# Kernel optimization log

Hardware: AMD Instinct MI355X
Metric: run time of the kernel (lower is better)

## Reference

```python
import jax, jax.numpy as jnp
import numpy as np

N_NODES = 50000


def _sage_max(x, src, dst, W_l, b_l, W_r):
    # gather neighbor (source) features, scatter-max to destination nodes
    msgs = x[src]                                   # [E, F]
    agg = jax.ops.segment_max(msgs, dst, num_segments=N_NODES)  # [N, F], -inf for empty
    agg = jnp.where(jnp.isneginf(agg), 0.0, agg)    # PyG fills isolated nodes with 0
    return agg @ W_l + b_l + x @ W_r                # lin_l(aggr) + lin_r(x)


def setup_inputs() -> dict:
    key = jax.random.key(0)
    ks = jax.random.split(key, 9)
    F_IN, H, OUT, E, EL = 128, 256, 32, 800000, 200000
    x = jax.random.normal(ks[0], (N_NODES, F_IN), dtype=jnp.float32)
    edge_index = jax.random.randint(ks[1], (2, E), 0, N_NODES, dtype=jnp.int64)
    edge_label_index = jax.random.randint(ks[2], (2, EL), 0, N_NODES, dtype=jnp.int64)
    s1 = 1.0 / np.sqrt(F_IN)
    s2 = 1.0 / np.sqrt(H)
    W1_l = jax.random.normal(ks[3], (F_IN, H), dtype=jnp.float32) * s1
    b1 = jnp.zeros((H,), dtype=jnp.float32)
    W1_r = jax.random.normal(ks[4], (F_IN, H), dtype=jnp.float32) * s1
    W2_l = jax.random.normal(ks[5], (H, OUT), dtype=jnp.float32) * s2
    b2 = jnp.zeros((OUT,), dtype=jnp.float32)
    W2_r = jax.random.normal(ks[6], (H, OUT), dtype=jnp.float32) * s2
    return {"x": x, "edge_index": edge_index, "edge_label_index": edge_label_index,
            "W1_l": W1_l, "b1": b1, "W1_r": W1_r,
            "W2_l": W2_l, "b2": b2, "W2_r": W2_r}


def reference(x, edge_index, edge_label_index, W1_l, b1, W1_r, W2_l, b2, W2_r):
    src, dst = edge_index[0], edge_index[1]
    # encode (eval mode: dropout is identity)
    h = jax.nn.relu(_sage_max(x, src, dst, W1_l, b1, W1_r))
    z = _sage_max(h, src, dst, W2_l, b2, W2_r)       # [N, 32]
    # decode: dot product between endpoint embeddings
    s = z[edge_label_index[0]]
    d = z[edge_label_index[1]]
    return jnp.sum(s * d, axis=-1)                   # [E_label]
```

## Files before the change

### kernel.cpp

```cpp
#include <hip/hip_runtime.h>
#include <hip/hip_bf16.h>
#include <math.h>

#define N_NODES 50000
#define NBKT 196
#define BSH 8
#define TILE2 4096
#define CAP 64
#define P2CAP 5888
#define SCAN_FLAG 0x40000000
#define ZSTRIDE 1600000

typedef __attribute__((ext_vector_type(8))) short short8;
typedef __attribute__((ext_vector_type(4))) float f32x4;

static __device__ __forceinline__ float b2f(unsigned int u16) {
    union { unsigned int i; float f; } c; c.i = u16 << 16; return c.f;
}
static __device__ __forceinline__ unsigned int fbits(float f) {
    union { float f; unsigned int i; } c; c.f = f; return c.i;
}
static __device__ __forceinline__ unsigned short f2b_rne(float f) {
    unsigned int u = fbits(f);
    u += 0x7fff + ((u >> 16) & 1);
    return (unsigned short)(u >> 16);
}

static __device__ __forceinline__ unsigned char quant8(float v) {
    int q = (int)(v * 15.9375f + 0.5f);
    return (unsigned char)min(q, 255);
}

static __device__ __forceinline__ unsigned char q8x(float v) {
    int q = __float2int_rn(v * 21.333334f) + 128;
    return (unsigned char)min(max(q, 0), 255);
}

static __device__ __forceinline__ short8 dq8(uint2 v8) {
    short8 r;
#pragma unroll
    for (int bi = 0; bi < 4; ++bi)
        r[bi] = (short)f2b_rne((float)((v8.x >> (8 * bi)) & 255u) * 0.0627451f);
#pragma unroll
    for (int bi = 0; bi < 4; ++bi)
        r[4 + bi] = (short)f2b_rne((float)((v8.y >> (8 * bi)) & 255u) * 0.0627451f);
    return r;
}

#define BYTEMAX16(V) do {                                                             \
    m[0]  = max(m[0],  (int)((V).x & 0xFF));                                          \
    m[1]  = max(m[1],  (int)(((V).x >> 8) & 0xFF));                                   \
    m[2]  = max(m[2],  (int)(((V).x >> 16) & 0xFF));                                  \
    m[3]  = max(m[3],  (int)((V).x >> 24));                                           \
    m[4]  = max(m[4],  (int)((V).y & 0xFF));                                          \
    m[5]  = max(m[5],  (int)(((V).y >> 8) & 0xFF));                                   \
    m[6]  = max(m[6],  (int)(((V).y >> 16) & 0xFF));                                  \
    m[7]  = max(m[7],  (int)((V).y >> 24));                                           \
    m[8]  = max(m[8],  (int)((V).z & 0xFF));                                          \
    m[9]  = max(m[9],  (int)(((V).z >> 8) & 0xFF));                                   \
    m[10] = max(m[10], (int)(((V).z >> 16) & 0xFF));                                  \
    m[11] = max(m[11], (int)((V).z >> 24));                                           \
    m[12] = max(m[12], (int)((V).w & 0xFF));                                          \
    m[13] = max(m[13], (int)(((V).w >> 8) & 0xFF));                                   \
    m[14] = max(m[14], (int)(((V).w >> 16) & 0xFF));                                  \
    m[15] = max(m[15], (int)((V).w >> 24));                                           \
} while (0)


__global__ __launch_bounds__(256) void k_prepbin(
        const float* __restrict__ x, unsigned short* __restrict__ xb,
        unsigned char* __restrict__ x8,
        const float* __restrict__ W1l, const float* __restrict__ W1r, unsigned short* __restrict__ wt1,
        const float* __restrict__ W2l, const float* __restrict__ W2r, unsigned short* __restrict__ wt2,
        const int* __restrict__ src, const int* __restrict__ dst, int E,
        uint2* __restrict__ tmp, int* __restrict__ cnts, int ntile) {
    __shared__ int cnt[256], sstart[256], lcur[256];
    __shared__ uint2 stage[TILE2];
    const int CX = (N_NODES * 128 / 4) / 256;
    const int CW = CX + 320;
    int b = blockIdx.x, t = threadIdx.x;
    if (b < CX) {
        int i = b * 256 + t;
        float4 v = *(const float4*)(x + (size_t)i * 4);
        ushort4 o;
        o.x = f2b_rne(v.x); o.y = f2b_rne(v.y); o.z = f2b_rne(v.z); o.w = f2b_rne(v.w);
        *(ushort4*)(xb + (size_t)i * 4) = o;
        uchar4 c8;
        c8.x = q8x(v.x); c8.y = q8x(v.y); c8.z = q8x(v.z); c8.w = q8x(v.w);
        *(uchar4*)(x8 + (size_t)i * 4) = c8;
    } else if (b < CX + 256) {
        int i = (b - CX) * 256 + t;
        int n = i >> 8, k = i & 255;
        float v = (k < 128) ? W1l[(size_t)k * 256 + n] : W1r[(size_t)(k - 128) * 256 + n];
        wt1[(size_t)n * 256 + k] = f2b_rne(v);
    } else if (b < CW) {
        int i = (b - CX - 256) * 256 + t;
        int n = i >> 9, k = i & 511;
        float v = (k < 256) ? W2l[(size_t)k * 32 + n] : W2r[(size_t)(k - 256) * 32 + n];
        wt2[(size_t)n * 512 + k] = f2b_rne(v);
    } else {
        int tb = b - CW;
        int e0 = tb * TILE2;
        int tilecnt = min(TILE2, E - e0);
        if (tilecnt <= 0) return;
        cnt[t] = 0;
        __syncthreads();
        if (tilecnt == TILE2) {
            for (int i = 4 * t; i < TILE2; i += 1024) {
                int4 d = *(const int4*)(dst + e0 + i);
                atomicAdd(&cnt[d.x >> BSH], 1);
                atomicAdd(&cnt[d.y >> BSH], 1);
                atomicAdd(&cnt[d.z >> BSH], 1);
                atomicAdd(&cnt[d.w >> BSH], 1);
            }
        } else {
            for (int i = t; i < tilecnt; i += 256)
                atomicAdd(&cnt[dst[e0 + i] >> BSH], 1);
        }
        __syncthreads();
        int cv = cnt[t];
        sstart[t] = cv;
        __syncthreads();
        for (int off = 1; off < 256; off <<= 1) {
            int add = (t >= off) ? sstart[t - off] : 0;
            __syncthreads();
            sstart[t] += add;
            __syncthreads();
        }
        int mystart = sstart[t] - cv;
        __syncthreads();
        sstart[t] = mystart;
        lcur[t] = mystart;
        __syncthreads();
        if (tilecnt == TILE2) {
            for (int i = 4 * t; i < TILE2; i += 1024) {
                int4 d = *(const int4*)(dst + e0 + i);
                int4 s = *(const int4*)(src + e0 + i);
                int q0 = atomicAdd(&lcur[d.x >> BSH], 1); stage[q0] = (uint2){(unsigned)s.x, (unsigned)d.x};
                int q1 = atomicAdd(&lcur[d.y >> BSH], 1); stage[q1] = (uint2){(unsigned)s.y, (unsigned)d.y};
                int q2 = atomicAdd(&lcur[d.z >> BSH], 1); stage[q2] = (uint2){(unsigned)s.z, (unsigned)d.z};
                int q3 = atomicAdd(&lcur[d.w >> BSH], 1); stage[q3] = (uint2){(unsigned)s.w, (unsigned)d.w};
            }
        } else {
            for (int i = t; i < tilecnt; i += 256) {
                int d = dst[e0 + i];
                int s = src[e0 + i];
                int q = atomicAdd(&lcur[d >> BSH], 1);
                uint2 p; p.x = (unsigned)s; p.y = (unsigned)d;
                stage[q] = p;
            }
        }
        __syncthreads();
        if (t < NBKT) cnts[(size_t)t * ntile + tb] = cnt[t];
        for (int i = t; i < tilecnt; i += 256) {
            uint2 p = stage[i];
            int bk = (int)(p.y >> BSH);
            tmp[((size_t)bk * ntile + tb) * CAP + (i - sstart[bk])] = p;
        }
    }
}


__global__ __launch_bounds__(256) void k_bin2(const uint2* __restrict__ tmp,
        const int* __restrict__ cnts, int* __restrict__ pub,
        int* __restrict__ rowptr, int* __restrict__ esrc, int N, int E, int ntile) {
    __shared__ int sc[256], toff[260], nodecnt[256], lcur[256];
    __shared__ int stage[P2CAP];
    __shared__ int shsum[4];
    int k = blockIdx.x, t = threadIdx.x;
    int grp = t >> 5, lane32 = t & 31;

    int c = (t < ntile) ? cnts[(size_t)k * ntile + t] : 0;
    sc[t] = c;
    __syncthreads();
    for (int off = 1; off < 256; off <<= 1) {
        int add = (t >= off) ? sc[t - off] : 0;
        __syncthreads();
        sc[t] += add;
        __syncthreads();
    }
    if (t < ntile) toff[t] = sc[t] - c;
    if (t == 255) toff[ntile] = sc[255];
    __syncthreads();
    int total = toff[ntile];

    if (t == 255) atomicExch(&pub[k], SCAN_FLAG | total);
    int v = 0;
    if (t < k) {
        int val;
        do { val = atomicOr(&pub[t], 0); } while (!(val & SCAN_FLAG) || (val & 0x80000000));
        v = val & (SCAN_FLAG - 1);
    }
#pragma unroll
    for (int off = 32; off >= 1; off >>= 1) v += __shfl_xor(v, off);
    if ((t & 63) == 0) shsum[t >> 6] = v;
    nodecnt[t] = 0;
    __syncthreads();
    int base = shsum[0] + shsum[1] + shsum[2] + shsum[3];

    for (int tile = grp; tile < ntile; tile += 8) {
        int tc = toff[tile + 1] - toff[tile];
        for (int e = lane32; e < tc; e += 32) {
            uint2 p = tmp[((size_t)k * ntile + tile) * CAP + e];
            atomicAdd(&nodecnt[(int)p.y & 255], 1);
        }
    }
    __syncthreads();

    int nc = nodecnt[t];
    sc[t] = nc;
    __syncthreads();
    for (int off = 1; off < 256; off <<= 1) {
        int add = (t >= off) ? sc[t - off] : 0;
        __syncthreads();
        sc[t] += add;
        __syncthreads();
    }
    int ex = sc[t] - nc;
    int node = (k << BSH) + t;
    if (node < N) rowptr[node] = base + ex;
    if (node == N) rowptr[N] = E;
    lcur[t] = ex;
    __syncthreads();

    if (total <= P2CAP) {
        for (int tile = grp; tile < ntile; tile += 8) {
            int tc = toff[tile + 1] - toff[tile];
            for (int e = lane32; e < tc; e += 32) {
                uint2 p = tmp[((size_t)k * ntile + tile) * CAP + e];
                int q = atomicAdd(&lcur[(int)p.y & 255], 1);
                stage[q] = (int)p.x;
            }
        }
        __syncthreads();
        for (int i = t; i < total; i += 256)
            esrc[base + i] = stage[i];
    } else {
        for (int tile = grp; tile < ntile; tile += 8) {
            int tc = toff[tile + 1] - toff[tile];
            for (int e = lane32; e < tc; e += 32) {
                uint2 p = tmp[((size_t)k * ntile + tile) * CAP + e];
                int q = atomicAdd(&lcur[(int)p.y & 255], 1);
                esrc[base + q] = (int)p.x;
            }
        }
    }
}


__global__ __launch_bounds__(256) void k_seg_max1(const unsigned char* __restrict__ feat8,
        const int* __restrict__ rowptr, const int* __restrict__ esrc,
        unsigned short* __restrict__ out) {
    int w = threadIdx.x >> 6, t = threadIdx.x & 63;
    int n = blockIdx.x * 4 + w;
    int lane8 = t & 7, sub = t >> 3;
    int beg = rowptr[n], end = rowptr[n + 1];
    int m[16];
#pragma unroll
    for (int k = 0; k < 16; ++k) m[k] = 0;
    for (int base = beg; base < end; base += 64) {
        int cnt = min(64, end - base);
        int vidx = (base + t < end) ? __builtin_nontemporal_load(&esrc[base + t]) : 0;
        for (int j = 0; j < cnt; j += 32) {
            int lim = cnt - j;
            if (lim > 16) {
                uint4 v[4];
#pragma unroll
                for (int u = 0; u < 4; ++u) {
                    int e = min(j + 8 * u + sub, cnt - 1);
                    int s = __shfl(vidx, e);
                    v[u] = *(const uint4*)(feat8 + (size_t)s * 128 + lane8 * 16);
                }
#pragma unroll
                for (int u = 0; u < 4; ++u) BYTEMAX16(v[u]);
            } else if (lim > 8) {
                uint4 v[2];
#pragma unroll
                for (int u = 0; u < 2; ++u) {
                    int e = min(j + 8 * u + sub, cnt - 1);
                    int s = __shfl(vidx, e);
                    v[u] = *(const uint4*)(feat8 + (size_t)s * 128 + lane8 * 16);
                }
#pragma unroll
                for (int u = 0; u < 2; ++u) BYTEMAX16(v[u]);
            } else {
                int e = min(j + sub, cnt - 1);
                int s = __shfl(vidx, e);
                uint4 v0 = *(const uint4*)(feat8 + (size_t)s * 128 + lane8 * 16);
                BYTEMAX16(v0);
            }
        }
    }
#pragma unroll
    for (int k = 0; k < 16; ++k) {
        m[k] = max(m[k], __shfl_xor(m[k], 8));
        m[k] = max(m[k], __shfl_xor(m[k], 16));
        m[k] = max(m[k], __shfl_xor(m[k], 32));
    }
    if (sub == 0) {
        unsigned int pk[8];
#pragma unroll
        for (int k = 0; k < 8; ++k) {
            float f0 = (beg == end) ? 0.f : (float)(m[2 * k]     - 128) * 0.046875f;
            float f1 = (beg == end) ? 0.f : (float)(m[2 * k + 1] - 128) * 0.046875f;
            pk[k] = (fbits(f0) >> 16) | (fbits(f1) & 0xffff0000u);
        }
        uint4 a, b;
        a.x = pk[0]; a.y = pk[1]; a.z = pk[2]; a.w = pk[3];
        b.x = pk[4]; b.y = pk[5]; b.z = pk[6]; b.w = pk[7];
        *(uint4*)(out + (size_t)n * 128 + lane8 * 16) = a;
        *(uint4*)(out + (size_t)n * 128 + lane8 * 16 + 8) = b;
    }
}


__global__ __launch_bounds__(256) void k_seg_max2(const unsigned char* __restrict__ feat8,
        const int* __restrict__ rowptr, const int* __restrict__ esrc,
        unsigned char* __restrict__ out8) {
    int w = threadIdx.x >> 6, t = threadIdx.x & 63;
    int n = blockIdx.x * 4 + w;
    int lane16 = t & 15, sub = t >> 4;
    int beg = rowptr[n], end = rowptr[n + 1];
    int m[16];
#pragma unroll
    for (int k = 0; k < 16; ++k) m[k] = 0;
    for (int base = beg; base < end; base += 64) {
        int cnt = min(64, end - base);
        int vidx = (base + t < end) ? __builtin_nontemporal_load(&esrc[base + t]) : 0;
        for (int j = 0; j < cnt; j += 32) {
            int lim = cnt - j;
            if (lim > 16) {
                uint4 v[8];
#pragma unroll
                for (int u = 0; u < 8; ++u) {
                    int e = min(j + 4 * u + sub, cnt - 1);
                    int s = __shfl(vidx, e);
                    v[u] = *(const uint4*)(feat8 + (size_t)s * 256 + lane16 * 16);
                }
#pragma unroll
                for (int u = 0; u < 8; ++u) BYTEMAX16(v[u]);
            } else if (lim > 8) {
                uint4 v[4];
#pragma unroll
                for (int u = 0; u < 4; ++u) {
                    int e = min(j + 4 * u + sub, cnt - 1);
                    int s = __shfl(vidx, e);
                    v[u] = *(const uint4*)(feat8 + (size_t)s * 256 + lane16 * 16);
                }
#pragma unroll
                for (int u = 0; u < 4; ++u) BYTEMAX16(v[u]);
            } else {
                uint4 v[2];
#pragma unroll
                for (int u = 0; u < 2; ++u) {
                    int e = min(j + 4 * u + sub, cnt - 1);
                    int s = __shfl(vidx, e);
                    v[u] = *(const uint4*)(feat8 + (size_t)s * 256 + lane16 * 16);
                }
#pragma unroll
                for (int u = 0; u < 2; ++u) BYTEMAX16(v[u]);
            }
        }
    }
#pragma unroll
    for (int k = 0; k < 16; ++k) {
        m[k] = max(m[k], __shfl_xor(m[k], 16));
        m[k] = max(m[k], __shfl_xor(m[k], 32));
    }
    if (sub == 0) {
        uint4 p;
        p.x = m[0]  | (m[1]  << 8) | (m[2]  << 16) | (m[3]  << 24);
        p.y = m[4]  | (m[5]  << 8) | (m[6]  << 16) | (m[7]  << 24);
        p.z = m[8]  | (m[9]  << 8) | (m[10] << 16) | (m[11] << 24);
        p.w = m[12] | (m[13] << 8) | (m[14] << 16) | (m[15] << 24);
        *(uint4*)(out8 + (size_t)n * 256 + lane16 * 16) = p;
    }
}


#define STAGE(bi, K0) do {                                                            \
    const unsigned short* Ab_ = ((K0) < 128) ? A0 : A1;                               \
    int kab_ = ((K0) & 127) * 2;                                                      \
    int kbb_ = (K0) * 2;                                                              \
    _Pragma("unroll")                                                                 \
    for (int ii = 0; ii < 2; ++ii) {                                                  \
        int c_ = ii * 256 + tid;                                                      \
        int r_ = c_ >> 2, gs_ = (c_ & 3) ^ (r_ & 3);                                  \
        const char* ga_ = (const char*)Ab_ + (size_t)(m0 + r_) * 256 + kab_ + gs_ * 16; \
        __builtin_amdgcn_global_load_lds(                                             \
            (const __attribute__((address_space(1))) void*)ga_,                       \
            (__attribute__((address_space(3))) void*)((char*)(SH + (bi) * 4096) + (ii * 256 + (tid & ~63)) * 16), \
            16, 0, 0);                                                                \
        const char* gb_ = (const char*)WT + (size_t)(n0 + r_) * 512 + kbb_ + gs_ * 16; \
        __builtin_amdgcn_global_load_lds(                                             \
            (const __attribute__((address_space(1))) void*)gb_,                       \
            (__attribute__((address_space(3))) void*)((char*)(SH + 12288 + (bi) * 4096) + (ii * 256 + (tid & ~63)) * 16), \
            16, 0, 0);                                                                \
    }                                                                                 \
} while (0)

#define VMCNT8() asm volatile("s_waitcnt vmcnt(8)" ::: "memory")
#define VMCNT6() asm volatile("s_waitcnt vmcnt(6)" ::: "memory")
#define VMCNT4() asm volatile("s_waitcnt vmcnt(4)" ::: "memory")
#define VMCNT3() asm volatile("s_waitcnt vmcnt(3)" ::: "memory")
#define VMCNT0() asm volatile("s_waitcnt vmcnt(0)" ::: "memory")
#define SBAR() do { __builtin_amdgcn_sched_barrier(0); __builtin_amdgcn_s_barrier(); __builtin_amdgcn_sched_barrier(0); } while (0)

#define COMPUTE(bi) do {                                                              \
    const short* Asb_ = SH + (bi) * 4096;                                             \
    const short* Bsb_ = SH + 12288 + (bi) * 4096;                                     \
    short8 a_[4], b_[4];                                                              \
    _Pragma("unroll")                                                                 \
    for (int i = 0; i < 4; ++i) {                                                     \
        int r_ = wr * 64 + i * 16 + lane16;                                           \
        a_[i] = *(const short8*)((const char*)Asb_ + r_ * 64 + ((q ^ (r_ & 3)) << 4)); \
    }                                                                                 \
    _Pragma("unroll")                                                                 \
    for (int j = 0; j < 4; ++j) {                                                     \
        int c_ = wc * 64 + j * 16 + lane16;                                           \
        b_[j] = *(const short8*)((const char*)Bsb_ + c_ * 64 + ((q ^ (c_ & 3)) << 4)); \
    }                                                                                 \
    _Pragma("unroll")                                                                 \
    for (int i = 0; i < 4; ++i)                                                       \
        _Pragma("unroll")                                                             \
        for (int j = 0; j < 4; ++j)                                                   \
            acc[i][j] = __builtin_amdgcn_mfma_f32_16x16x32_bf16(a_[i], b_[j], acc[i][j], 0, 0, 0); \
} while (0)

__global__ __launch_bounds__(256) void k_lin1_mfma(
        const unsigned short* __restrict__ A0, const unsigned short* __restrict__ A1,
        const unsigned short* __restrict__ WT, const float* __restrict__ bias,
        const unsigned short* __restrict__ WT2, float* __restrict__ zpart,
        unsigned char* __restrict__ H8, int M) {
    __shared__ __align__(16) short SH[24576];
    short* Hs = SH;

    int tid = threadIdx.x;
    int m0 = blockIdx.y * 128, n0 = blockIdx.x * 128;
    int L = tid & 63, wv = tid >> 6;
    int wr = wv >> 1, wc = wv & 1;
    int lane16 = L & 15, q = L >> 4;

    f32x4 acc[4][4];
#pragma unroll
    for (int i = 0; i < 4; ++i)
#pragma unroll
        for (int j = 0; j < 4; ++j) acc[i][j] = (f32x4){0.f, 0.f, 0.f, 0.f};

    STAGE(0, 0);
    STAGE(1, 32);
    STAGE(2, 64);

    VMCNT8(); SBAR(); COMPUTE(0); SBAR(); STAGE(0, 96);
    VMCNT8(); SBAR(); COMPUTE(1); SBAR(); STAGE(1, 128);
    VMCNT8(); SBAR(); COMPUTE(2); SBAR(); STAGE(2, 160);
    VMCNT8(); SBAR(); COMPUTE(0); SBAR(); STAGE(0, 192);
    VMCNT8(); SBAR(); COMPUTE(1); SBAR(); STAGE(1, 224);
    VMCNT8(); SBAR(); COMPUTE(2);
    VMCNT4(); SBAR(); COMPUTE(0);
    VMCNT0(); SBAR(); COMPUTE(1);

    __syncthreads();

#pragma unroll
    for (int i = 0; i < 4; ++i) {
#pragma unroll
        for (int r = 0; r < 4; ++r) {
            int lrow = wr * 64 + i * 16 + q * 4 + r;
            int row = m0 + lrow;
#pragma unroll
            for (int j = 0; j < 4; ++j) {
                int lcol = wc * 64 + j * 16 + lane16;
                int col = n0 + lcol;
                float v = fmaxf(acc[i][j][r] + bias[col], 0.f);
                Hs[lrow * 136 + lcol] = (short)f2b_rne(v);
                if (row < M) H8[(size_t)row * 256 + col] = quant8(v);
            }
        }
    }
    __syncthreads();

    f32x4 acc2[2][2];
#pragma unroll
    for (int i = 0; i < 2; ++i)
#pragma unroll
        for (int j = 0; j < 2; ++j) acc2[i][j] = (f32x4){0.f, 0.f, 0.f, 0.f};
#pragma unroll
    for (int kk = 0; kk < 4; ++kk) {
        short8 a2[2], b2[2];
#pragma unroll
        for (int i = 0; i < 2; ++i)
            a2[i] = *(const short8*)&Hs[(wv * 32 + i * 16 + lane16) * 136 + kk * 32 + q * 8];
#pragma unroll
        for (int j = 0; j < 2; ++j)
            b2[j] = *(const short8*)(WT2 + (size_t)(j * 16 + lane16) * 512 + 256 + n0 + kk * 32 + q * 8);
#pragma unroll
        for (int i = 0; i < 2; ++i)
#pragma unroll
            for (int j = 0; j < 2; ++j)
                acc2[i][j] = __builtin_amdgcn_mfma_f32_16x16x32_bf16(a2[i], b2[j], acc2[i][j], 0, 0, 0);
    }
    float* zp = zpart + (size_t)blockIdx.x * ZSTRIDE;
#pragma unroll
    for (int i = 0; i < 2; ++i) {
#pragma unroll
        for (int r = 0; r < 4; ++r) {
            int row = m0 + wv * 32 + i * 16 + q * 4 + r;
            if (row >= M) continue;
#pragma unroll
            for (int j = 0; j < 2; ++j) {
                int col = j * 16 + lane16;
                zp[(size_t)row * 32 + col] = acc2[i][j][r];
            }
        }
    }
}


#define STAGE2(bi, T) do {                                                            \
    _Pragma("unroll")                                                                 \
    for (int ii = 0; ii < 2; ++ii) {                                                  \
        int off_ = (ii * 256 + tid) * 16;                                             \
        int r_ = off_ >> 6, c_ = off_ & 63;                                           \
        const char* ga_ = (const char*)A8 + (size_t)(m0 + r_) * 256 + (T) * 64 + c_;  \
        __builtin_amdgcn_global_load_lds(                                             \
            (const __attribute__((address_space(1))) void*)ga_,                       \
            (__attribute__((address_space(3))) void*)(SH8 + (bi) * 8192 + (ii * 256 + (tid & ~63)) * 16), \
            16, 0, 0);                                                                \
    }                                                                                 \
    {                                                                                 \
        int off_ = tid * 16;                                                          \
        int r_ = off_ >> 7, c_ = off_ & 127;                                          \
        const char* gb_ = (const char*)WT + (size_t)r_ * 1024 + (T) * 128 + c_;       \
        __builtin_amdgcn_global_load_lds(                                             \
            (const __attribute__((address_space(1))) void*)gb_,                       \
            (__attribute__((address_space(3))) void*)(SH8 + 24576 + (bi) * 4096 + (tid & ~63) * 16), \
            16, 0, 0);                                                                \
    }                                                                                 \
} while (0)

#define COMPUTE2(bi) do {                                                             \
    const unsigned char* As_ = (const unsigned char*)SH8 + (bi) * 8192;               \
    const char* Bs_ = SH8 + 24576 + (bi) * 4096;                                      \
    _Pragma("unroll")                                                                 \
    for (int kk = 0; kk < 64; kk += 32) {                                             \
        short8 a_[2], b_[2];                                                          \
        _Pragma("unroll")                                                             \
        for (int i = 0; i < 2; ++i) {                                                 \
            uint2 va_ = *(const uint2*)(As_ + (wv * 32 + i * 16 + lane16) * 64 + kk + q * 8); \
            a_[i] = dq8(va_);                                                         \
        }                                                                             \
        _Pragma("unroll")                                                             \
        for (int j = 0; j < 2; ++j)                                                   \
            b_[j] = *(const short8*)(Bs_ + (j * 16 + lane16) * 128 + (kk + q * 8) * 2); \
        _Pragma("unroll")                                                             \
        for (int i = 0; i < 2; ++i)                                                   \
            _Pragma("unroll")                                                         \
            for (int j = 0; j < 2; ++j)                                               \
                acc[i][j] = __builtin_amdgcn_mfma_f32_16x16x32_bf16(a_[i], b_[j], acc[i][j], 0, 0, 0); \
    }                                                                                 \
} while (0)

__global__ __launch_bounds__(256) void k_lin2_mfma(
        const unsigned char* __restrict__ A8,
        const unsigned short* __restrict__ WT, const float* __restrict__ bias,
        const float* __restrict__ zpart, float* __restrict__ Z, int M) {
    __shared__ __align__(16) char SH8[36864];

    int tid = threadIdx.x;
    int m0 = blockIdx.x * 128;
    int L = tid & 63, wv = tid >> 6;
    int lane16 = L & 15, q = L >> 4;

    f32x4 acc[2][2];
#pragma unroll
    for (int i = 0; i < 2; ++i)
#pragma unroll
        for (int j = 0; j < 2; ++j) acc[i][j] = (f32x4){0.f, 0.f, 0.f, 0.f};

    STAGE2(0, 0);
    STAGE2(1, 1);
    STAGE2(2, 2);

    VMCNT6(); SBAR(); COMPUTE2(0); SBAR(); STAGE2(0, 3);
    VMCNT6(); SBAR(); COMPUTE2(1);
    VMCNT3(); SBAR(); COMPUTE2(2);
    VMCNT0(); SBAR(); COMPUTE2(0);

#pragma unroll
    for (int i = 0; i < 2; ++i) {
#pragma unroll
        for (int r = 0; r < 4; ++r) {
            int row = m0 + wv * 32 + i * 16 + q * 4 + r;
            if (row >= M) continue;
#pragma unroll
            for (int j = 0; j < 2; ++j) {
                int col = j * 16 + lane16;
                float zp = zpart[(size_t)row * 32 + col]
                         + zpart[(size_t)ZSTRIDE + (size_t)row * 32 + col];
                Z[(size_t)row * 32 + col] = acc[i][j][r] + bias[col] + zp;
            }
        }
    }
}


__global__ void k_decode(const float* __restrict__ z, const int* __restrict__ eli,
                         int EL, float* __restrict__ out) {
    int tid = blockIdx.x * blockDim.x + threadIdx.x;
    int e = tid >> 3, lane = tid & 7;
    if (e >= EL) return;
    int s = eli[e], d = eli[EL + e];
    float4 a = *((const float4*)(z + (size_t)s * 32) + lane);
    float4 b = *((const float4*)(z + (size_t)d * 32) + lane);
    float dot = a.x * b.x + a.y * b.y + a.z * b.z + a.w * b.w;
    dot += __shfl_xor(dot, 1);
    dot += __shfl_xor(dot, 2);
    dot += __shfl_xor(dot, 4);
    if (lane == 0) out[e] = dot;
}


extern "C" void kernel_launch(void* const* d_in, const int* in_sizes, int n_in,
                              void* d_out, int out_size, void* d_ws, size_t ws_size,
                              hipStream_t stream) {
    const float* x   = (const float*)d_in[0];
    const int*   ei  = (const int*)d_in[1];
    const int*   eli = (const int*)d_in[2];
    const float* W1l = (const float*)d_in[3];
    const float* b1  = (const float*)d_in[4];
    const float* W1r = (const float*)d_in[5];
    const float* W2l = (const float*)d_in[6];
    const float* b2  = (const float*)d_in[7];
    const float* W2r = (const float*)d_in[8];
    float* out = (float*)d_out;

    int N  = N_NODES;
    int E  = in_sizes[1] / 2;
    int EL = in_sizes[2] / 2;
    const int* src = ei;
    const int* dst = ei + E;

    char* ws = (char*)d_ws;
    size_t off = 0;
    auto alloc = [&](size_t bytes) -> void* {
        void* p = ws + off;
        off += (bytes + 255) & ~(size_t)255;
        return p;
    };
    unsigned short* xb   = (unsigned short*)alloc((size_t)N * 128 * 2);
    unsigned char*  x8   = (unsigned char*)alloc((size_t)N * 128);
    unsigned short* aggb = (unsigned short*)alloc((size_t)(N + 128) * 256 * 2);
    unsigned char*  h8   = (unsigned char*)alloc((size_t)N * 256);
    float* zbuf          = (float*)alloc((size_t)N * 32 * 4);
    float* zpart         = (float*)alloc((size_t)2 * ZSTRIDE * 4);
    unsigned short* wt1  = (unsigned short*)alloc(256 * 256 * 2);
    unsigned short* wt2  = (unsigned short*)alloc(32 * 512 * 2);
    int* rowptr   = (int*)alloc((size_t)(N + 1) * 4);
    int ntile     = (E + TILE2 - 1) / TILE2;
    int* cnts     = (int*)alloc((size_t)NBKT * ntile * 4);
    int* pub      = (int*)alloc(256 * 4);
    int* esrc     = (int*)alloc((size_t)E * 4);
    uint2* tmpp   = (uint2*)aggb;
    unsigned char* agg8 = (unsigned char*)aggb;

    const int tb = 256;
    const int CW = 6250 + 320;

    k_prepbin<<<CW + ntile, tb, 0, stream>>>(x, xb, x8, W1l, W1r, wt1, W2l, W2r, wt2,
                                             src, dst, E, tmpp, cnts, ntile);
    k_bin2<<<NBKT, tb, 0, stream>>>(tmpp, cnts, pub, rowptr, esrc, N, E, ntile);

    k_seg_max1<<<(N + 3) / 4, tb, 0, stream>>>(x8, rowptr, esrc, aggb);
    dim3 g1(2, (N + 127) / 128);
    k_lin1_mfma<<<g1, tb, 0, stream>>>(aggb, xb, wt1, b1, wt2, zpart, h8, N);

    k_seg_max2<<<(N + 3) / 4, tb, 0, stream>>>(h8, rowptr, esrc, agg8);
    k_lin2_mfma<<<(N + 127) / 128, tb, 0, stream>>>(agg8, wt2, b2, zpart, zbuf, N);

    k_decode<<<(EL * 8 + 255) / 256, tb, 0, stream>>>(zbuf, eli, EL, out);
}
```

Baseline: 222.0 us.

## Give each wave private LDS staging to remove block barriers in lin1 GEMM

The lin1 MFMA GEMM now has each wave load its own A rows and B columns into a private LDS region, double-buffered, instead of sharing a block-wide triple buffer. The main loop synchronises with per-wave vmcnt/lgkmcnt waits and no s_barrier. The cost is redundant global loads, since A and B tiles are fetched twice across waves, and LDS use rises to 64KB, which may lower occupancy.

```diff
diff --git a/kernel.cpp b/kernel.cpp
--- a/kernel.cpp
+++ b/kernel.cpp
@@ -378,47 +378,43 @@
 }
 
 
-#define STAGE(bi, K0) do {                                                            \
+#define WVM8() do { asm volatile("s_waitcnt vmcnt(8)" ::: "memory"); __builtin_amdgcn_sched_barrier(0); } while (0)
+#define WVM0() do { asm volatile("s_waitcnt vmcnt(0)" ::: "memory"); __builtin_amdgcn_sched_barrier(0); } while (0)
+#define WLG0() do { asm volatile("s_waitcnt lgkmcnt(0)" ::: "memory"); __builtin_amdgcn_sched_barrier(0); } while (0)
+
+#define WSTAGE(b, K0) do {                                                            \
     const unsigned short* Ab_ = ((K0) < 128) ? A0 : A1;                               \
     int kab_ = ((K0) & 127) * 2;                                                      \
-    int kbb_ = (K0) * 2;                                                              \
     _Pragma("unroll")                                                                 \
-    for (int ii = 0; ii < 2; ++ii) {                                                  \
-        int c_ = ii * 256 + tid;                                                      \
-        int r_ = c_ >> 2, gs_ = (c_ & 3) ^ (r_ & 3);                                  \
-        const char* ga_ = (const char*)Ab_ + (size_t)(m0 + r_) * 256 + kab_ + gs_ * 16; \
+    for (int ii = 0; ii < 4; ++ii) {                                                  \
+        int rr_ = ii * 16 + (L >> 2);                                                 \
+        int gs_ = (L & 3) ^ (rr_ & 3);                                                \
+        const char* ga_ = (const char*)Ab_ + (size_t)(m0 + wr * 64 + rr_) * 256 + kab_ + gs_ * 16; \
         __builtin_amdgcn_global_load_lds(                                             \
             (const __attribute__((address_space(1))) void*)ga_,                       \
-            (__attribute__((address_space(3))) void*)((char*)(SH + (bi) * 4096) + (ii * 256 + (tid & ~63)) * 16), \
+            (__attribute__((address_space(3))) void*)(SH8 + wvb + (b) * 8192 + ii * 1024), \
             16, 0, 0);                                                                \
-        const char* gb_ = (const char*)WT + (size_t)(n0 + r_) * 512 + kbb_ + gs_ * 16; \
+        const char* gb_ = (const char*)WT + (size_t)(n0 + wc * 64 + rr_) * 512 + (K0) * 2 + gs_ * 16; \
         __builtin_amdgcn_global_load_lds(                                             \
             (const __attribute__((address_space(1))) void*)gb_,                       \
-            (__attribute__((address_space(3))) void*)((char*)(SH + 12288 + (bi) * 4096) + (ii * 256 + (tid & ~63)) * 16), \
+            (__attribute__((address_space(3))) void*)(SH8 + wvb + (b) * 8192 + 4096 + ii * 1024), \
             16, 0, 0);                                                                \
     }                                                                                 \
 } while (0)
 
-#define VMCNT8() asm volatile("s_waitcnt vmcnt(8)" ::: "memory")
-#define VMCNT6() asm volatile("s_waitcnt vmcnt(6)" ::: "memory")
-#define VMCNT4() asm volatile("s_waitcnt vmcnt(4)" ::: "memory")
-#define VMCNT3() asm volatile("s_waitcnt vmcnt(3)" ::: "memory")
-#define VMCNT0() asm volatile("s_waitcnt vmcnt(0)" ::: "memory")
-#define SBAR() do { __builtin_amdgcn_sched_barrier(0); __builtin_amdgcn_s_barrier(); __builtin_amdgcn_sched_barrier(0); } while (0)
-
-#define COMPUTE(bi) do {                                                              \
-    const short* Asb_ = SH + (bi) * 4096;                                             \
-    const short* Bsb_ = SH + 12288 + (bi) * 4096;                                     \
+#define WCOMP(b) do {                                                                 \
+    const char* As_ = SH8 + wvb + (b) * 8192;                                         \
+    const char* Bs_ = As_ + 4096;                                                     \
     short8 a_[4], b_[4];                                                              \
     _Pragma("unroll")                                                                 \
     for (int i = 0; i < 4; ++i) {                                                     \
-        int r_ = wr * 64 + i * 16 + lane16;                                           \
-        a_[i] = *(const short8*)((const char*)Asb_ + r_ * 64 + ((q ^ (r_ & 3)) << 4)); \
+        int r_ = i * 16 + lane16;                                                     \
+        a_[i] = *(const short8*)(As_ + r_ * 64 + ((q ^ (r_ & 3)) << 4));              \
     }                                                                                 \
     _Pragma("unroll")                                                                 \
     for (int j = 0; j < 4; ++j) {                                                     \
-        int c_ = wc * 64 + j * 16 + lane16;                                           \
-        b_[j] = *(const short8*)((const char*)Bsb_ + c_ * 64 + ((q ^ (c_ & 3)) << 4)); \
+        int c_ = j * 16 + lane16;                                                     \
+        b_[j] = *(const short8*)(Bs_ + c_ * 64 + ((q ^ (c_ & 3)) << 4));              \
     }                                                                                 \
     _Pragma("unroll")                                                                 \
     for (int i = 0; i < 4; ++i)                                                       \
@@ -432,14 +428,15 @@
         const unsigned short* __restrict__ WT, const float* __restrict__ bias,
         const unsigned short* __restrict__ WT2, float* __restrict__ zpart,
         unsigned char* __restrict__ H8, int M) {
-    __shared__ __align__(16) short SH[24576];
-    short* Hs = SH;
+    __shared__ __align__(16) char SH8[65536];
+    short* Hs = (short*)SH8;
 
     int tid = threadIdx.x;
     int m0 = blockIdx.y * 128, n0 = blockIdx.x * 128;
     int L = tid & 63, wv = tid >> 6;
     int wr = wv >> 1, wc = wv & 1;
     int lane16 = L & 15, q = L >> 4;
+    int wvb = wv * 16384;
 
     f32x4 acc[4][4];
 #pragma unroll
@@ -447,18 +444,16 @@
 #pragma unroll
         for (int j = 0; j < 4; ++j) acc[i][j] = (f32x4){0.f, 0.f, 0.f, 0.f};
 
-    STAGE(0, 0);
-    STAGE(1, 32);
-    STAGE(2, 64);
-
-    VMCNT8(); SBAR(); COMPUTE(0); SBAR(); STAGE(0, 96);
-    VMCNT8(); SBAR(); COMPUTE(1); SBAR(); STAGE(1, 128);
-    VMCNT8(); SBAR(); COMPUTE(2); SBAR(); STAGE(2, 160);
-    VMCNT8(); SBAR(); COMPUTE(0); SBAR(); STAGE(0, 192);
-    VMCNT8(); SBAR(); COMPUTE(1); SBAR(); STAGE(1, 224);
-    VMCNT8(); SBAR(); COMPUTE(2);
-    VMCNT4(); SBAR(); COMPUTE(0);
-    VMCNT0(); SBAR(); COMPUTE(1);
+    WSTAGE(0, 0);
+    WSTAGE(1, 32);
+    WVM8(); WCOMP(0); WLG0(); WSTAGE(0, 64);
+    WVM8(); WCOMP(1); WLG0(); WSTAGE(1, 96);
+    WVM8(); WCOMP(0); WLG0(); WSTAGE(0, 128);
+    WVM8(); WCOMP(1); WLG0(); WSTAGE(1, 160);
+    WVM8(); WCOMP(0); WLG0(); WSTAGE(0, 192);
+    WVM8(); WCOMP(1); WLG0(); WSTAGE(1, 224);
+    WVM8(); WCOMP(0);
+    WVM0(); WCOMP(1);
 
     __syncthreads();
 
@@ -516,6 +511,11 @@
     }
 }
 
+
+#define VMCNT6() asm volatile("s_waitcnt vmcnt(6)" ::: "memory")
+#define VMCNT3() asm volatile("s_waitcnt vmcnt(3)" ::: "memory")
+#define VMCNT0() asm volatile("s_waitcnt vmcnt(0)" ::: "memory")
+#define SBAR() do { __builtin_amdgcn_sched_barrier(0); __builtin_amdgcn_s_barrier(); __builtin_amdgcn_sched_barrier(0); } while (0)
 
 #define STAGE2(bi, T) do {                                                            \
     _Pragma("unroll")                                                                 \
```

Result: no change. 224.3 us (+1.0%).
